# Kernel tuning notes

Hardware: AMD Instinct MI355X
Metric: run time of the kernel (lower is better)

## Reference

```python
import jax, jax.numpy as jnp
import numpy as np

FEATS = [(100, 100), (50, 50), (25, 25), (13, 13)]  # (W, H) per level
BS, NQ, D = 2, 10000, 256
NH, NL, NP, G = 8, 4, 4, 8
HD = D // NH


def grid_sample_bilinear(im, grid):
    """torch.nn.functional.grid_sample(mode='bilinear', padding_mode='zeros', align_corners=False).
    im: [N, C, H, W]; grid: [N, Hg, Wg, 2] in [-1, 1] (x, y). Returns [N, C, Hg, Wg]."""
    N, C, H, W = im.shape
    Hg, Wg = grid.shape[1], grid.shape[2]
    x = (grid[..., 0] + 1.0) * (W * 0.5) - 0.5
    y = (grid[..., 1] + 1.0) * (H * 0.5) - 0.5
    x0 = jnp.floor(x); y0 = jnp.floor(y)
    wx1 = x - x0; wx0 = 1.0 - wx1
    wy1 = y - y0; wy0 = 1.0 - wy1
    imf = im.reshape(N, C, H * W)

    def corner(xi, yi, w):
        inb = (xi >= 0) & (xi < W) & (yi >= 0) & (yi < H)
        xi_c = jnp.clip(xi, 0, W - 1).astype(jnp.int32)
        yi_c = jnp.clip(yi, 0, H - 1).astype(jnp.int32)
        idx = (yi_c * W + xi_c).reshape(N, 1, Hg * Wg)
        vals = jnp.take_along_axis(imf, idx, axis=2).reshape(N, C, Hg, Wg)
        return vals * (w * inb.astype(im.dtype))[:, None]

    out = (corner(x0, y0, wx0 * wy0) + corner(x0 + 1, y0, wx1 * wy0)
           + corner(x0, y0 + 1, wx0 * wy1) + corner(x0 + 1, y0 + 1, wx1 * wy1))
    return out


def setup_inputs() -> dict:
    key = jax.random.key(0)
    ks = jax.random.split(key, 7)
    nv = sum(w * h for (w, h) in FEATS)
    return {
        "query": jax.random.normal(ks[0], (BS, NQ, D), jnp.float32),
        "value": jax.random.normal(ks[1], (BS, nv, NH, HD), jnp.float32),
        "reference_points": jax.random.uniform(ks[2], (BS, NQ, NL, 2), jnp.float32),
        "spatial_shapes": jnp.array(FEATS, jnp.float32),  # rows are (W, H)
        "W_off": jax.random.normal(ks[3], (NH * NL * NP * 2, D), jnp.float32) * 0.02,
        "b_off": jax.random.normal(ks[4], (NH * NL * NP * 2,), jnp.float32) * 0.5,
        "W_attn": jax.random.normal(ks[5], (NH * NL * NP, D), jnp.float32) * 0.02,
        "b_attn": jax.random.normal(ks[6], (NH * NL * NP,), jnp.float32) * 0.02,
    }


def reference(query, value, reference_points, spatial_shapes, W_off, b_off, W_attn, b_attn):
    bs, nq, _ = query.shape
    # sampling offsets: [bs, nq, NH, NL*NP*2] with (level, point, xy) layout
    off = (jnp.einsum('bqd,od->bqo', query, W_off) + b_off).reshape(bs, nq, NH, NL * NP * 2)
    # reference points tiled to the same (level, point, xy) layout
    ref = jnp.broadcast_to(reference_points[:, :, None, :, None, :],
                           (bs, nq, NH, NL, NP, 2)).reshape(bs, nq, NH, NL * NP * 2)
    # offset normalizer: (1/W, 1/H) per level, tiled over points
    inv = 1.0 / spatial_shapes  # [NL, 2]
    norm = jnp.broadcast_to(inv[:, None, :], (NL, NP, 2)).reshape(-1)
    loc = (ref + off * norm) * 2.0 - 1.0  # [bs, nq, NH, NL*NP*2]
    loc = loc.reshape(bs, nq, NH, NL, NP, 2)

    # attention weights: softmax over (NL*NP), then rearranged to [bs*NH, 1, nq/G, NL*G*NP]
    aw = jax.nn.softmax((jnp.einsum('bqd,od->bqo', query, W_attn) + b_attn)
                        .reshape(bs, nq, NH, NL * NP), axis=-1)
    aw = aw.reshape(bs, nq // G, G, NH, NL, NP).transpose(0, 3, 1, 4, 2, 5)
    aw = aw.reshape(bs * NH, 1, nq // G, NL * G * NP)

    # per-level grid_sample
    sizes = [w * h for (w, h) in FEATS]
    starts = np.concatenate([[0], np.cumsum(sizes)]).tolist()
    sampled = []
    for lvl, (Wl, Hl) in enumerate(FEATS):
        val_l = value[:, starts[lvl]:starts[lvl + 1]]  # [bs, Hl*Wl, NH, HD]
        val_l = val_l.transpose(0, 2, 3, 1).reshape(bs * NH, HD, Hl, Wl)
        grid_l = loc[:, :, :, lvl].transpose(0, 2, 1, 3, 4)  # [bs, NH, nq, NP, 2]
        grid_l = grid_l.reshape(bs * NH, nq // G, G * NP, 2)
        sampled.append(grid_sample_bilinear(val_l, grid_l))  # [bs*NH, HD, nq/G, G*NP]
    sv = jnp.concatenate(sampled, axis=-1)  # [bs*NH, HD, nq/G, NL*G*NP]

    out = sv * aw
    # reduce_sum linear (fixed 0/1 weight from init_weights) == sum over levels and points per group slot
    out = out.reshape(bs * NH, HD, nq // G, NL, G, NP).sum(axis=(3, 5))  # [bs*NH, HD, nq/G, G]
    return out.reshape(bs, NH * HD, nq)
```

## Files before the change

### kernel.cpp

```cpp
#include <hip/hip_runtime.h>

#define NQ   10000
#define BSZ  2
#define DIM  256
#define NH   8
#define HD   32
#define NLV  4
#define NPT  4
#define NV   13294
#define MT   (BSZ*NQ)
#define NOUT 384
#define NVAL (BSZ*NV*NH*HD)
#define GEMM_BLOCKS 939
#define PREP_BLOCKS 6647
#define QPB  16

typedef float    floatx4 __attribute__((ext_vector_type(4)));
typedef int      intx4   __attribute__((ext_vector_type(4)));
typedef __bf16   bf16x8  __attribute__((ext_vector_type(8)));
typedef _Float16 halfx8  __attribute__((ext_vector_type(8)));
typedef _Float16 halfx4  __attribute__((ext_vector_type(4)));
typedef _Float16 halfx2  __attribute__((ext_vector_type(2)));

__device__ __forceinline__ unsigned pk_bf16(float lo, float hi) {
  return __builtin_amdgcn_perm(__float_as_uint(hi) + 0x8000u,
                               __float_as_uint(lo) + 0x8000u, 0x07060302);
}

__device__ __forceinline__ unsigned short f32_to_f16_bits(float f) {
  _Float16 h = (_Float16)f;
  return __builtin_bit_cast(unsigned short, h);
}

__global__ __launch_bounds__(256) void gp_kernel(
    const float* __restrict__ query, const float* __restrict__ W_off,
    const float* __restrict__ W_attn,
    const float* __restrict__ b_off, const float* __restrict__ b_attn,
    const float* __restrict__ value,
    _Float16* __restrict__ rawh, _Float16* __restrict__ vf16) {
  const int bid = blockIdx.x;
  const int tid = threadIdx.x;
  if (bid >= GEMM_BLOCKS) {
    int i = (bid - GEMM_BLOCKS) * 256 + tid;
    if (i * 4 < NVAL) {
      floatx4 v = *(const floatx4*)&value[i * 4];
      halfx4 t = { (_Float16)v.x, (_Float16)v.y, (_Float16)v.z, (_Float16)v.w };
      *(uint2*)&vf16[i * 4] = *(const uint2*)&t;
    }
    return;
  }
  __shared__ unsigned short As[64][40];
  __shared__ unsigned short Bs[128][40];
  const int n0 = (bid % 3) * 128;
  const int m0 = (bid / 3) * 64;
  const int wave = tid >> 6;
  const int lane = tid & 63;
  const int quad = lane >> 4;
  const int l16  = lane & 15;
  floatx4 acc[8] = {};
  const int ar = tid >> 2;
  const int ac = (tid & 3) * 8;
  const int br = tid >> 1;
  const int bc = (tid & 1) * 16;
  const float* __restrict__ Wsrc =
      (n0 < 256) ? (W_off + (size_t)n0 * DIM) : (W_attn + (size_t)(n0 - 256) * DIM);

  for (int k0 = 0; k0 < DIM; k0 += 32) {
    {
      int gm = m0 + ar;
      floatx4 a0 = {}, a1 = {};
      if (gm < MT) {
        const float* src = query + (size_t)gm * DIM + k0 + ac;
        a0 = *(const floatx4*)src;
        a1 = *(const floatx4*)(src + 4);
      }
      uint4 ua = { pk_bf16(a0.x, a0.y), pk_bf16(a0.z, a0.w),
                   pk_bf16(a1.x, a1.y), pk_bf16(a1.z, a1.w) };
      *(uint4*)&As[ar][ac] = ua;
    }
    {
      const float* src = Wsrc + (size_t)br * DIM + k0 + bc;
      floatx4 b0 = *(const floatx4*)src;
      floatx4 b1 = *(const floatx4*)(src + 4);
      floatx4 b2 = *(const floatx4*)(src + 8);
      floatx4 b3 = *(const floatx4*)(src + 12);
      uint4 u0 = { pk_bf16(b0.x, b0.y), pk_bf16(b0.z, b0.w),
                   pk_bf16(b1.x, b1.y), pk_bf16(b1.z, b1.w) };
      uint4 u1 = { pk_bf16(b2.x, b2.y), pk_bf16(b2.z, b2.w),
                   pk_bf16(b3.x, b3.y), pk_bf16(b3.z, b3.w) };
      *(uint4*)&Bs[br][bc]     = u0;
      *(uint4*)&Bs[br][bc + 8] = u1;
    }
    __syncthreads();
    bf16x8 a = *(const bf16x8*)&As[wave*16 + l16][quad*8];
    #pragma unroll
    for (int nt = 0; nt < 8; nt++) {
      bf16x8 b = *(const bf16x8*)&Bs[nt*16 + l16][quad*8];
      acc[nt] = __builtin_amdgcn_mfma_f32_16x16x32_bf16(a, b, acc[nt], 0, 0, 0);
    }
    __syncthreads();
  }
  #pragma unroll
  for (int nt = 0; nt < 8; nt++) {
    int gn = n0 + nt*16 + l16;
    float bias = (gn < 256) ? b_off[gn] : b_attn[gn - 256];
    #pragma unroll
    for (int r = 0; r < 4; r++) {
      int gm = m0 + wave*16 + quad*4 + r;
      if (gm < MT) rawh[(size_t)gm*NOUT + gn] = (_Float16)(acc[nt][r] + bias);
    }
  }
}

union SampleSmem {
  uint4 pk[16 * 128];
  float tr[16 * 260];
};

__global__ __launch_bounds__(256, 5) void sample_kernel(
    const _Float16* __restrict__ rawh, const _Float16* __restrict__ vf16,
    const float* __restrict__ refp, float* __restrict__ out) {
  const int b  = blockIdx.y;
  const int q0 = blockIdx.x * QPB;
  const int mbase = b * NQ + q0;
  const int tid = threadIdx.x;

  __shared__ SampleSmem sm;

  constexpr int WLI[4] = {100, 50, 25, 13};
  constexpr int STI[4] = {0, 10000, 12500, 13125};

  const int p  = tid & 3;
  const int r4 = tid >> 2;

  #pragma unroll
  for (int half = 0; half < 2; ++half) {
    const int row = half * 64 + r4;
    const int hh  = row & 7;
    const int ql0 = row >> 3;
    const int m   = mbase + ql0;
    const _Float16* rp = rawh + (size_t)m * NOUT;

    float lg[4], rpx[4], rpy[4];
    #pragma unroll
    for (int it = 0; it < 4; ++it) {
      unsigned oxy = *(const unsigned*)(rp + hh*32 + it*8 + p*2);
      halfx2 o2 = __builtin_bit_cast(halfx2, oxy);
      lg[it] = (float)rp[256 + hh*16 + it*4 + p];
      float Wl = (float)WLI[it];
      float rx = refp[((size_t)m*NLV + it)*2 + 0];
      float ry = refp[((size_t)m*NLV + it)*2 + 1];
      rpx[it] = rx * Wl + (float)o2.x - 0.5f;
      rpy[it] = ry * Wl + (float)o2.y - 0.5f;
    }

    float mx = fmaxf(fmaxf(lg[0], lg[1]), fmaxf(lg[2], lg[3]));
    mx = fmaxf(mx, __shfl_xor(mx, 1));
    mx = fmaxf(mx, __shfl_xor(mx, 2));
    float e[4], sden = 0.f;
    #pragma unroll
    for (int it = 0; it < 4; ++it) { e[it] = __expf(lg[it] - mx); sden += e[it]; }
    sden += __shfl_xor(sden, 1);
    sden += __shfl_xor(sden, 2);
    float inv = 1.f / sden;

    #pragma unroll
    for (int it = 0; it < 4; ++it) {
      float aw = e[it] * inv;
      float px = rpx[it], py = rpy[it];
      float x0f = floorf(px), y0f = floorf(py);
      int x0 = (int)x0f, y0 = (int)y0f;
      float wx1 = px - x0f, wx0 = 1.f - wx1;
      float wy1 = py - y0f, wy0 = 1.f - wy1;
      const int Wl = WLI[it], STl = STI[it];
      unsigned short ib[4], wb[4];
      #pragma unroll
      for (int t = 0; t < 4; ++t) {
        int xi = x0 + (t & 1), yi = y0 + (t >> 1);
        bool inb = (xi >= 0) & (xi < Wl) & (yi >= 0) & (yi < Wl);
        ib[t] = inb ? (unsigned short)(STl + yi*Wl + xi) : (unsigned short)0;
        float w = inb ? (aw * ((t & 1) ? wx1 : wx0) * ((t >> 1) ? wy1 : wy0)) : 0.f;
        wb[t] = f32_to_f16_bits(w);
      }
      uint4 pk = { (unsigned)ib[0] | ((unsigned)ib[1] << 16),
                   (unsigned)ib[2] | ((unsigned)ib[3] << 16),
                   (unsigned)wb[0] | ((unsigned)wb[1] << 16),
                   (unsigned)wb[2] | ((unsigned)wb[3] << 16) };
      sm.pk[(it*4 + p)*128 + row] = pk;
    }
  }
  __syncthreads();

  const int wv = tid >> 6, lane = tid & 63;
  const int qh = lane >> 5;
  const int h  = (lane >> 2) & 7, cq = lane & 3;
  const char* vbh = (const char*)vf16 + (size_t)b * (NV*NH*HD*2) + h*64 + cq*16;
  floatx4 accs[2][2];
  #pragma unroll
  for (int pass = 0; pass < 2; ++pass) {
    const int ql   = wv*4 + pass*2 + qh;
    const int rowb = ql*8 + h;
    floatx4 a0 = {0.f,0.f,0.f,0.f}, a1 = {0.f,0.f,0.f,0.f};
    #pragma unroll 4
    for (int pt = 0; pt < 16; ++pt) {
      uint4 pk = sm.pk[pt*128 + rowb];
      uint2 wpair = { pk.z, pk.w };
      halfx4 hw = __builtin_bit_cast(halfx4, wpair);
      int o0 = (int)(pk.x & 0xffffu) << 9;
      int o1 = (int)(pk.x >> 16)     << 9;
      int o2 = (int)(pk.y & 0xffffu) << 9;
      int o3 = (int)(pk.y >> 16)     << 9;
      halfx8 v0 = *(const halfx8*)(vbh + o0);
      halfx8 v1 = *(const halfx8*)(vbh + o1);
      halfx8 v2 = *(const halfx8*)(vbh + o2);
      halfx8 v3 = *(const halfx8*)(vbh + o3);
      #pragma unroll
      for (int t = 0; t < 4; ++t) {
        halfx8 v = (t==0) ? v0 : (t==1) ? v1 : (t==2) ? v2 : v3;
        _Float16 wt = hw[t];
        a0.x += (float)wt * (float)v[0];
        a0.y += (float)wt * (float)v[1];
        a0.z += (float)wt * (float)v[2];
        a0.w += (float)wt * (float)v[3];
        a1.x += (float)wt * (float)v[4];
        a1.y += (float)wt * (float)v[5];
        a1.z += (float)wt * (float)v[6];
        a1.w += (float)wt * (float)v[7];
      }
    }
    accs[pass][0] = a0;
    accs[pass][1] = a1;
  }
  __syncthreads();

  #pragma unroll
  for (int pass = 0; pass < 2; ++pass) {
    const int ql  = wv*4 + pass*2 + qh;
    const int ch0 = h*32 + cq*8;
    *(floatx4*)&sm.tr[ql*260 + ch0]     = accs[pass][0];
    *(floatx4*)&sm.tr[ql*260 + ch0 + 4] = accs[pass][1];
  }
  __syncthreads();
  {
    const int ch = tid;
    float vals[QPB];
    #pragma unroll
    for (int q = 0; q < QPB; ++q) vals[q] = sm.tr[q*260 + ch];
    float* op = out + ((size_t)b*DIM + ch)*NQ + q0;
    *(floatx4*)&op[0]  = *(const floatx4*)&vals[0];
    *(floatx4*)&op[4]  = *(const floatx4*)&vals[4];
    *(floatx4*)&op[8]  = *(const floatx4*)&vals[8];
    *(floatx4*)&op[12] = *(const floatx4*)&vals[12];
  }
}

extern "C" void kernel_launch(void* const* d_in, const int* in_sizes, int n_in,
                              void* d_out, int out_size, void* d_ws, size_t ws_size,
                              hipStream_t stream) {
  const float* query  = (const float*)d_in[0];
  const float* value  = (const float*)d_in[1];
  const float* refp   = (const float*)d_in[2];
  const float* W_off  = (const float*)d_in[4];
  const float* b_off  = (const float*)d_in[5];
  const float* W_attn = (const float*)d_in[6];
  const float* b_attn = (const float*)d_in[7];
  float* out = (float*)d_out;

  char* ws = (char*)d_ws;
  _Float16* rawh = (_Float16*)ws;
  _Float16* vf16 = (_Float16*)(ws + 15360000);

  hipLaunchKernelGGL(gp_kernel, dim3(GEMM_BLOCKS + PREP_BLOCKS), dim3(256), 0, stream,
                     query, W_off, W_attn, b_off, b_attn, value, rawh, vf16);
  hipLaunchKernelGGL(sample_kernel, dim3(NQ / QPB, BSZ), dim3(256), 0, stream,
                     rawh, vf16, refp, out);
}
```

Baseline: 170.5 us.

## Store clamped base index per sample and remap blocks across XCDs

Each sample point now stores one clamped 2x2 base index plus the row stride instead of four separate corner indices. Weights are reassigned so an out-of-range corner gets zero weight, which lets the gather derive the other three addresses by fixed offsets and shrinks the shared-memory record. The shared arrays are split into index and weight planes padded to 130 rows, presumably to cut bank conflicts. The 2D grid is flattened into a 1D grid with an XCD-aware block remap so neighbouring query tiles land on the same XCD and share L2. Occupancy hint rises from 5 to 6 blocks per CU, at the cost of register pressure and a more intricate clamp-and-weight computation.

After: 165.5 us. 2.9% less time.

```diff
diff --git a/kernel.cpp b/kernel.cpp
--- a/kernel.cpp
+++ b/kernel.cpp
@@ -14,6 +14,7 @@
 #define GEMM_BLOCKS 939
 #define PREP_BLOCKS 6647
 #define QPB  16
+#define SROW 130
 
 typedef float    floatx4 __attribute__((ext_vector_type(4)));
 typedef int      intx4   __attribute__((ext_vector_type(4)));
@@ -113,15 +114,19 @@
 }
 
 union SampleSmem {
-  uint4 pk[16 * 128];
+  struct { unsigned i[16 * SROW]; uint2 w[16 * SROW]; } s;
   float tr[16 * 260];
 };
 
-__global__ __launch_bounds__(256, 5) void sample_kernel(
+__global__ __launch_bounds__(256, 6) void sample_kernel(
     const _Float16* __restrict__ rawh, const _Float16* __restrict__ vf16,
     const float* __restrict__ refp, float* __restrict__ out) {
-  const int b  = blockIdx.y;
-  const int q0 = blockIdx.x * QPB;
+  const int orig = blockIdx.x;
+  const int xcd  = orig & 7;
+  const int rep  = orig >> 3;
+  const int wg   = (xcd < 2 ? xcd * 157 : 2 * 157 + (xcd - 2) * 156) + rep;
+  const int b  = wg / 625;
+  const int q0 = (wg % 625) * QPB;
   const int mbase = b * NQ + q0;
   const int tid = threadIdx.x;
 
@@ -173,20 +178,22 @@
       float wx1 = px - x0f, wx0 = 1.f - wx1;
       float wy1 = py - y0f, wy0 = 1.f - wy1;
       const int Wl = WLI[it], STl = STI[it];
-      unsigned short ib[4], wb[4];
-      #pragma unroll
-      for (int t = 0; t < 4; ++t) {
-        int xi = x0 + (t & 1), yi = y0 + (t >> 1);
-        bool inb = (xi >= 0) & (xi < Wl) & (yi >= 0) & (yi < Wl);
-        ib[t] = inb ? (unsigned short)(STl + yi*Wl + xi) : (unsigned short)0;
-        float w = inb ? (aw * ((t & 1) ? wx1 : wx0) * ((t >> 1) ? wy1 : wy0)) : 0.f;
-        wb[t] = f32_to_f16_bits(w);
-      }
-      uint4 pk = { (unsigned)ib[0] | ((unsigned)ib[1] << 16),
-                   (unsigned)ib[2] | ((unsigned)ib[3] << 16),
-                   (unsigned)wb[0] | ((unsigned)wb[1] << 16),
-                   (unsigned)wb[2] | ((unsigned)wb[3] << 16) };
-      sm.pk[(it*4 + p)*128 + row] = pk;
+      int xb = min(max(x0, 0), Wl - 2);
+      int yb = min(max(y0, 0), Wl - 2);
+      float wxn0 = (xb == x0) ? wx0 : (xb == x0 + 1) ? wx1 : 0.f;
+      float wxn1 = (xb == x0) ? wx1 : (xb == x0 - 1) ? wx0 : 0.f;
+      float wyn0 = (yb == y0) ? wy0 : (yb == y0 + 1) ? wy1 : 0.f;
+      float wyn1 = (yb == y0) ? wy1 : (yb == y0 - 1) ? wy0 : 0.f;
+      unsigned idx0 = (unsigned)(STl + yb * Wl + xb);
+      unsigned short w00 = f32_to_f16_bits(aw * wxn0 * wyn0);
+      unsigned short w01 = f32_to_f16_bits(aw * wxn1 * wyn0);
+      unsigned short w10 = f32_to_f16_bits(aw * wxn0 * wyn1);
+      unsigned short w11 = f32_to_f16_bits(aw * wxn1 * wyn1);
+      const int pt = it*4 + p;
+      sm.s.i[pt*SROW + row] = idx0 | ((unsigned)Wl << 16);
+      uint2 wp = { (unsigned)w00 | ((unsigned)w01 << 16),
+                   (unsigned)w10 | ((unsigned)w11 << 16) };
+      sm.s.w[pt*SROW + row] = wp;
     }
   }
   __syncthreads();
@@ -203,17 +210,17 @@
     floatx4 a0 = {0.f,0.f,0.f,0.f}, a1 = {0.f,0.f,0.f,0.f};
     #pragma unroll 4
     for (int pt = 0; pt < 16; ++pt) {
-      uint4 pk = sm.pk[pt*128 + rowb];
-      uint2 wpair = { pk.z, pk.w };
-      halfx4 hw = __builtin_bit_cast(halfx4, wpair);
-      int o0 = (int)(pk.x & 0xffffu) << 9;
-      int o1 = (int)(pk.x >> 16)     << 9;
-      int o2 = (int)(pk.y & 0xffffu) << 9;
-      int o3 = (int)(pk.y >> 16)     << 9;
-      halfx8 v0 = *(const halfx8*)(vbh + o0);
-      halfx8 v1 = *(const halfx8*)(vbh + o1);
-      halfx8 v2 = *(const halfx8*)(vbh + o2);
-      halfx8 v3 = *(const halfx8*)(vbh + o3);
+      unsigned iw = sm.s.i[pt*SROW + rowb];
+      uint2 wp   = sm.s.w[pt*SROW + rowb];
+      halfx4 hw = __builtin_bit_cast(halfx4, wp);
+      int o0   = (int)(iw & 0xffffu) << 9;
+      int orow = (int)(iw >> 16)     << 9;
+      const char* p0 = vbh + o0;
+      const char* p2 = p0 + orow;
+      halfx8 v0 = *(const halfx8*)(p0);
+      halfx8 v1 = *(const halfx8*)(p0 + 512);
+      halfx8 v2 = *(const halfx8*)(p2);
+      halfx8 v3 = *(const halfx8*)(p2 + 512);
       #pragma unroll
       for (int t = 0; t < 4; ++t) {
         halfx8 v = (t==0) ? v0 : (t==1) ? v1 : (t==2) ? v2 : v3;
@@ -272,6 +279,6 @@
 
   hipLaunchKernelGGL(gp_kernel, dim3(GEMM_BLOCKS + PREP_BLOCKS), dim3(256), 0, stream,
                      query, W_off, W_attn, b_off, b_attn, value, rawh, vf16);
-  hipLaunchKernelGGL(sample_kernel, dim3(NQ / QPB, BSZ), dim3(256), 0, stream,
+  hipLaunchKernelGGL(sample_kernel, dim3(2 * (NQ / QPB)), dim3(256), 0, stream,
                      rawh, vf16, refp, out);
 }
```
